# Kernel tuning notes

Hardware: AMD Instinct MI355X
Metric: run time of the kernel (lower is better)

The kernel has to match this reference:

```python
import jax, jax.numpy as jnp
import numpy as np

# NTM hyperparams (must match init_kwargs)
U = 256        # controller units
N = 128        # memory locations
M = 64         # memory vector size
R = 1          # read heads
WH = 1         # write heads
SHIFT = 1      # conv shift range
S = 2 * SHIFT + 1
OUT = 8        # num_bits_per_vector
CLIP = 20.0
IN_DIM = OUT + 1  # copy task input channels
H = R + WH
PER = M + 1 + 1 + S + 1           # k, beta, g, s, gamma per head
P = H * PER + WH * 2 * M          # + erase/add per write head


def setup_inputs() -> dict:
    key = jax.random.key(0)
    ks = jax.random.split(key, 10)
    B, T = 128, 130
    ctrl_in = IN_DIM + R * M
    def gn(k, shape, fan_in):
        return jax.random.normal(k, shape, jnp.float32) / jnp.sqrt(jnp.float32(fan_in))
    return {
        "inputs": (jax.random.uniform(ks[0], (B, T, IN_DIM)) > 0.5).astype(jnp.float32),
        "W_x": gn(ks[1], (ctrl_in, 4 * U), ctrl_in),
        "W_h": gn(ks[2], (U, 4 * U), U),
        "b_lstm": jnp.zeros((4 * U,), jnp.float32),
        "W_p": gn(ks[3], (U, P), U),
        "b_p": jnp.zeros((P,), jnp.float32),
        "W_o": gn(ks[4], (U + R * M, OUT), U + R * M),
        "b_o": jnp.zeros((OUT,), jnp.float32),
        "r0": jax.random.normal(ks[5], (R, M), jnp.float32) * 0.1,
        "w0": jax.random.normal(ks[6], (H, N), jnp.float32) * 0.1,
        "max_seq_len": 64,
    }


def _ntm_forward(inputs, W_x, W_h, b_lstm, W_p, b_p, W_o, b_o, r0, w0):
    B, T, _ = inputs.shape
    # constant-init memory, learned init read vectors / weightings
    Mem0 = jnp.full((B, N, M), 1e-6, jnp.float32)
    r_prev0 = jnp.broadcast_to(jnp.tanh(r0)[None], (B, R, M))
    w_prev0 = jnp.broadcast_to(jax.nn.softmax(w0, axis=-1)[None], (B, H, N))
    h0 = jnp.zeros((B, U), jnp.float32)
    c0 = jnp.zeros((B, U), jnp.float32)

    def step(carry, x_t):
        h, c, r_prev, w_prev, Mem = carry
        # controller LSTM (input = x_t ++ prev read vectors)
        ctrl_in = jnp.concatenate([x_t, r_prev.reshape(B, R * M)], axis=-1)
        gates = ctrl_in @ W_x + h @ W_h + b_lstm
        i, f, g_, o = jnp.split(gates, 4, axis=-1)
        c = jax.nn.sigmoid(f) * c + jax.nn.sigmoid(i) * jnp.tanh(g_)
        h = jax.nn.sigmoid(o) * jnp.tanh(c)
        # head parameters
        params = jnp.clip(h @ W_p + b_p, -CLIP, CLIP)
        hp = params[:, : H * PER].reshape(B, H, PER)
        k = jnp.tanh(hp[..., :M])                              # [B,H,M]
        beta = jax.nn.softplus(hp[..., M])[..., None]          # [B,H,1]
        g = jax.nn.sigmoid(hp[..., M + 1])[..., None]          # [B,H,1]
        s = jax.nn.softmax(hp[..., M + 2 : M + 2 + S], axis=-1)  # [B,H,S]
        gamma = (1.0 + jax.nn.softplus(hp[..., M + 2 + S]))[..., None]  # [B,H,1]
        ea = params[:, H * PER :].reshape(B, WH, 2, M)
        erase = jax.nn.sigmoid(ea[:, :, 0])                    # [B,WH,M]
        add = jnp.tanh(ea[:, :, 1])                            # [B,WH,M]
        # content addressing: cosine similarity
        inner = jnp.einsum("bhm,bnm->bhn", k, Mem)
        kn = jnp.linalg.norm(k, axis=-1, keepdims=True)        # [B,H,1]
        Mn = jnp.linalg.norm(Mem, axis=-1)[:, None, :]         # [B,1,N]
        K = inner / (kn * Mn + 1e-8)
        w_c = jax.nn.softmax(beta * K, axis=-1)                # [B,H,N]
        # interpolation
        w_g = g * w_c + (1.0 - g) * w_prev
        # circular convolutional shift
        w_tilde = jnp.zeros_like(w_g)
        for d in range(-SHIFT, SHIFT + 1):
            w_tilde = w_tilde + s[..., d + SHIFT : d + SHIFT + 1] * jnp.roll(w_g, d, axis=-1)
        # sharpening
        w_pow = w_tilde ** gamma
        w = w_pow / (jnp.sum(w_pow, axis=-1, keepdims=True) + 1e-8)
        w_r, w_w = w[:, :R], w[:, R:]
        # write (sequential over write heads)
        for j in range(WH):
            ww = w_w[:, j, :, None]                            # [B,N,1]
            Mem = Mem * (1.0 - ww * erase[:, j, None, :]) + ww * add[:, j, None, :]
        # read
        r = jnp.einsum("brn,bnm->brm", w_r, Mem)
        out = jnp.clip(jnp.concatenate([h, r.reshape(B, R * M)], axis=-1) @ W_o + b_o, -CLIP, CLIP)
        return (h, c, r, w, Mem), out

    xs = jnp.swapaxes(inputs, 0, 1)  # [T,B,IN]
    _, outs = jax.lax.scan(step, (h0, c0, r_prev0, w_prev0, Mem0), xs)
    return jnp.swapaxes(outs, 0, 1)  # [B,T,OUT]


def reference(inputs, W_x, W_h, b_lstm, W_p, b_p, W_o, b_o, r0, w0, max_seq_len):
    seq = _ntm_forward(inputs, W_x, W_h, b_lstm, W_p, b_p, W_o, b_o, r0, w0)
    logits = seq[:, max_seq_len + 1 :, :]  # copy task slice
    return jax.nn.sigmoid(logits)
```

## Files before the change

kernel.cpp:

```cpp
#include <hip/hip_runtime.h>
#include <math.h>

typedef _Float16 h2_t __attribute__((ext_vector_type(2)));

#define U_ 256
#define NN 128
#define MM 64
#define OUT_ 8
#define CLIPV 20.0f
#define IN_DIM_ 9
#define PP 268
#define B_ 128
#define T_ 130
#define TSTART 65

#define NWXI 6144
#define NWH8 16384
#define NWP8 4352
#define WXI_OFF 0
#define WH8_OFF 98304
#define WP8_OFF 360448
#define BLH_OFF 430080
#define BPP_OFF 434176
#define COMM_OFF 435264
#define COMM_STRIDE 2176
#define COMM_SZ (B_*COMM_STRIDE)
#define PREP_N (NWXI + NWH8 + NWP8 + 256 + 272)

#define WSCALE 256.f
#define HSCALE 127.f
#define OSCALE (1.f/(256.f*127.f))

__device__ __forceinline__ float sigf(float x){ return 1.0f/(1.0f+__expf(-x)); }
__device__ __forceinline__ float splus(float x){ return log1pf(__expf(x)); }
__device__ __forceinline__ float clipf(float x){ return fminf(fmaxf(x,-CLIPV),CLIPV); }

#if defined(__has_builtin)
#if __has_builtin(__builtin_amdgcn_sdot4)
#define SDOT4(a,b,c) __builtin_amdgcn_sdot4((a),(b),(c),false)
#endif
#endif
#ifndef SDOT4
__device__ __forceinline__ int sdot4_sw(int a, int b, int c){
    c += (int)(signed char)(a      ) * (int)(signed char)(b      );
    c += (int)(signed char)(a >> 8 ) * (int)(signed char)(b >> 8 );
    c += (int)(signed char)(a >> 16) * (int)(signed char)(b >> 16);
    c += (a >> 24) * (b >> 24);
    return c;
}
#define SDOT4(a,b,c) sdot4_sw((a),(b),(c))
#endif

#define SD4(u, hw) { \
    a0 = SDOT4((int)(u).x, hw, a0); a1 = SDOT4((int)(u).y, hw, a1); \
    a2 = SDOT4((int)(u).z, hw, a2); a3 = SDOT4((int)(u).w, hw, a3); }
#define SD4P(u, hw) { \
    pa0 = SDOT4((int)(u).x, hw, pa0); pa1 = SDOT4((int)(u).y, hw, pa1); \
    pa2 = SDOT4((int)(u).z, hw, pa2); pa3 = SDOT4((int)(u).w, hw, pa3); }

__device__ __forceinline__ unsigned ei8(float w){
    int v = (int)rintf(w * WSCALE);
    v = v < -127 ? -127 : (v > 127 ? 127 : v);
    return (unsigned)(v & 0xFF);
}

__device__ __forceinline__ unsigned packi8x4(float a, float b, float c, float d){
    int va = (int)rintf(a * HSCALE); va = va < -127 ? -127 : (va > 127 ? 127 : va);
    int vb = (int)rintf(b * HSCALE); vb = vb < -127 ? -127 : (vb > 127 ? 127 : vb);
    int vc = (int)rintf(c * HSCALE); vc = vc < -127 ? -127 : (vc > 127 ? 127 : vc);
    int vd = (int)rintf(d * HSCALE); vd = vd < -127 ? -127 : (vd > 127 ? 127 : vd);
    return (va & 0xFF) | ((vb & 0xFF) << 8) | ((vc & 0xFF) << 16) | ((vd & 0xFF) << 24);
}

__global__ void prep_kernel(const float* __restrict__ W_x, const float* __restrict__ W_h,
                            const float* __restrict__ W_p, const float* __restrict__ b_lstm,
                            const float* __restrict__ b_p,
                            uint4* __restrict__ wxi8, uint4* __restrict__ whi8,
                            uint4* __restrict__ wpi8,
                            float4* __restrict__ blh, float* __restrict__ bpp)
{
    for (int idx = blockIdx.x*blockDim.x + threadIdx.x; idx < PREP_N; idx += gridDim.x*blockDim.x){
        if (idx < NWXI){
            int hf = idx/3072, rem = idx - hf*3072;
            int wv = rem/192, r2 = rem - wv*192, j = r2>>6, ln = r2&63;
            int g4 = wv*8 + (ln>>3), q = ln&7, kb = q*12 + 4*j;
            unsigned c[4];
            #pragma unroll
            for (int g=0; g<4; ++g){
                int col = g*256 + hf*128 + g4;
                unsigned w = 0;
                #pragma unroll
                for (int k=0; k<4; ++k){
                    int K = kb+k;
                    float f = (K<64) ? W_x[(9+K)*1024+col] : (K<73 ? W_x[(K-64)*1024+col] : 0.f);
                    w |= ei8(f) << (8*k);
                }
                c[g] = w;
            }
            wxi8[idx] = make_uint4(c[0],c[1],c[2],c[3]);
        } else if (idx < NWXI + NWH8){
            int e = idx - NWXI;
            int hf = e>>13, rem = e&8191, g4 = rem>>6, s = rem&63;
            int j = s>>3, q = s&7, kb = q*32 + 4*j;
            unsigned c[4];
            #pragma unroll
            for (int g=0; g<4; ++g){
                int col = g*256 + hf*128 + g4;
                c[g] = ei8(W_h[(kb+0)*1024+col])
                     | (ei8(W_h[(kb+1)*1024+col]) << 8)
                     | (ei8(W_h[(kb+2)*1024+col]) << 16)
                     | (ei8(W_h[(kb+3)*1024+col]) << 24);
            }
            whi8[e] = make_uint4(c[0],c[1],c[2],c[3]);
        } else if (idx < NWXI + NWH8 + NWP8){
            int e = idx - NWXI - NWH8;
            int cg = e>>6, s = e&63;
            int j = s>>3, q = s&7, kb = q*32 + 4*j;
            unsigned c[4];
            #pragma unroll
            for (int g=0; g<4; ++g){
                int cl = cg*4+g;
                if (cl < PP){
                    c[g] = ei8(W_p[(kb+0)*PP+cl])
                         | (ei8(W_p[(kb+1)*PP+cl]) << 8)
                         | (ei8(W_p[(kb+2)*PP+cl]) << 16)
                         | (ei8(W_p[(kb+3)*PP+cl]) << 24);
                } else c[g] = 0u;
            }
            wpi8[e] = make_uint4(c[0],c[1],c[2],c[3]);
        } else if (idx < NWXI + NWH8 + NWP8 + 256){
            int u = idx - NWXI - NWH8 - NWP8;
            blh[u] = make_float4(b_lstm[u], b_lstm[256+u], b_lstm[512+u], b_lstm[768+u]);
        } else {
            int j = idx - NWXI - NWH8 - NWP8 - 256;
            bpp[j] = (j < PP) ? b_p[j] : 0.f;
        }
    }
}

__device__ __forceinline__ float decodeP(int rc, float p){
    if (rc < 64 || (rc >= 70 && rc < 134) || rc >= 204) return tanhf(p);
    if (rc >= 140 && rc < 204) return sigf(p);
    return p;
}

__global__ __launch_bounds__(1024,1) void ntm_kernel(
    const float* __restrict__ inputs,
    const float* __restrict__ W_o, const float* __restrict__ b_o,
    const float* __restrict__ r0, const float* __restrict__ w0,
    const uint4* __restrict__ wxi8, const uint4* __restrict__ whi8,
    const uint4* __restrict__ wpi8,
    const float4* __restrict__ blh, const float* __restrict__ bpp,
    char* comm, float* __restrict__ out)
{
    const int bid = blockIdx.x, hf = bid>>7, b = bid&127;
    const int t = threadIdx.x, wv = t>>6, ln = t&63;
    const int g4 = t>>3, q = t&7;

    char* cb = comm + b*COMM_STRIDE;
    volatile float* hOwn = (volatile float*)(cb + hf*512);
    volatile float* hOth = (volatile float*)(cb + (hf^1)*512);
    volatile int*   flg  = (volatile int*)(cb + 2112);

    __shared__ uint4 wxL8[3072];
    __shared__ uint4 whL8[4][1024];
    __shared__ float Mem[NN][MM+1];
    __shared__ float4 gpart4[128];
    __shared__ float4 blhL[128];
    __shared__ float hbuf[U_];
    __shared__ float cbuf[128];
    __shared__ unsigned hq[64];
    __shared__ unsigned xq[24];
    __shared__ float prmS[12];
    __shared__ float scal[12];
    __shared__ float kv[2][MM], ebuf[MM], abuf[MM];
    __shared__ float innr[2][NN], Mn[NN], wgs[2][NN], wtab[2][NN];
    __shared__ float rpart[16][MM];
    __shared__ float jpart[OUT_];

    for (int i=t; i<3072; i+=1024) wxL8[i] = wxi8[hf*3072 + i];
    for (int i=t; i<4096; i+=1024){
        int j = i>>10, jj = i&1023;
        whL8[j][jj] = whi8[hf*8192 + (jj>>3)*64 + j*8 + (jj&7)];
    }
    for (int i=t; i<NN*MM; i+=1024) Mem[i>>6][i&63] = 1e-6f;
    if (t < 128){
        gpart4[t] = make_float4(0.f,0.f,0.f,0.f);
        blhL[t] = blh[hf*128+t];
        cbuf[t] = 0.f;
        Mn[t] = 8e-6f;
    }
    if (t < 64) hq[t] = 0u;
    if (t < U_) hbuf[t] = 0.f;
    if (t >= 128 && t < 256){
        int h = (t-128)>>6, l = t&63;
        float v0 = w0[h*NN + l], v1 = w0[h*NN + l + 64];
        float mx = fmaxf(v0,v1);
        for (int off=32; off>=1; off>>=1) mx = fmaxf(mx, __shfl_xor(mx, off));
        float e0 = __expf(v0-mx), e1 = __expf(v1-mx);
        float s = e0+e1;
        for (int off=32; off>=1; off>>=1) s += __shfl_xor(s, off);
        wtab[h][l] = e0/s; wtab[h][l+64] = e1/s;
    }
    if (t >= 256 && t < 280){
        int p = t-256;
        if (p < 16){
            xq[p] = packi8x4(tanhf(r0[4*p]), tanhf(r0[4*p+1]), tanhf(r0[4*p+2]), tanhf(r0[4*p+3]));
        } else if (p < 19){
            const float* xin = inputs + b*T_*IN_DIM_;
            int e0 = 4*(p-16);
            float f0 = (e0+0<IN_DIM_) ? xin[e0+0] : 0.f;
            float f1 = (e0+1<IN_DIM_) ? xin[e0+1] : 0.f;
            float f2 = (e0+2<IN_DIM_) ? xin[e0+2] : 0.f;
            float f3 = (e0+3<IN_DIM_) ? xin[e0+3] : 0.f;
            xq[p] = packi8x4(f0,f1,f2,f3);
        } else xq[p] = 0u;
    }
    __syncthreads();

    for (int step=0; step<T_; ++step){
        const int* xqi = (const int*)xq;

        {
            const uint4* wb = wxL8 + wv*192;
            int a0=0,a1=0,a2=0,a3=0;
            #pragma unroll
            for (int j=0; j<3; ++j){
                uint4 u = wb[j*64 + ln];
                int xw = xqi[q*3+j];
                SD4(u, xw);
            }
            #pragma unroll
            for (int m=1; m<8; m<<=1){
                a0 += __shfl_xor(a0,m); a1 += __shfl_xor(a1,m);
                a2 += __shfl_xor(a2,m); a3 += __shfl_xor(a3,m);
            }
            if (q==0){
                float4 bb = blhL[g4]; float4 gp = gpart4[g4];
                float gi=a0*OSCALE+bb.x+gp.x, gf=a1*OSCALE+bb.y+gp.y;
                float gg=a2*OSCALE+bb.z+gp.z, go=a3*OSCALE+bb.w+gp.w;
                float c = sigf(gf)*cbuf[g4] + sigf(gi)*tanhf(gg);
                cbuf[g4] = c;
                float h = sigf(go)*tanhf(c);
                hbuf[hf*128+g4] = h;
                hOwn[g4] = h;
            }
        }
        __syncthreads();
        if (t==0){
            flg[hf] = step+1;
            while (flg[hf^1] < step+1) __builtin_amdgcn_s_sleep(2);
        }
        __syncthreads();
        if (t < 128){
            hbuf[(hf^1)*128 + t] = hOth[t];
        } else if (t < 160){
            const int jj = t-128;
            const float* hp = &hbuf[hf*128 + 4*jj];
            hq[hf*32 + jj] = packi8x4(hp[0], hp[1], hp[2], hp[3]);
        } else if (t < 192){
            const int jj = t-160;
            float h0 = hOth[4*jj], h1 = hOth[4*jj+1], h2 = hOth[4*jj+2], h3 = hOth[4*jj+3];
            hq[(hf^1)*32 + jj] = packi8x4(h0, h1, h2, h3);
        }
        __syncthreads();

        const int* hqi = (const int*)hq;

        {
            const uint4* wrow = whi8 + hf*8192 + g4*64;
            int a0=0,a1=0,a2=0,a3=0;
            uint4 s4 = wrow[32+q], s5 = wrow[40+q], s6 = wrow[48+q], s7 = wrow[56+q];
            uint4 l0 = whL8[0][t], l1 = whL8[1][t], l2 = whL8[2][t], l3 = whL8[3][t];
            int hw0=hqi[q*8+0], hw1=hqi[q*8+1], hw2=hqi[q*8+2], hw3=hqi[q*8+3];
            int hw4=hqi[q*8+4], hw5=hqi[q*8+5], hw6=hqi[q*8+6], hw7=hqi[q*8+7];
            SD4(l0, hw0); SD4(l1, hw1);
            SD4(l2, hw2); SD4(l3, hw3);
            SD4(s4, hw4); SD4(s5, hw5);
            SD4(s6, hw6); SD4(s7, hw7);
            #pragma unroll
            for (int m=1; m<8; m<<=1){
                a0 += __shfl_xor(a0,m); a1 += __shfl_xor(a1,m);
                a2 += __shfl_xor(a2,m); a3 += __shfl_xor(a3,m);
            }
            if (q==0) gpart4[g4] = make_float4(a0*OSCALE, a1*OSCALE, a2*OSCALE, a3*OSCALE);
        }
        if (t < 544){
            const int cg = t>>3, qq = t&7;
            const uint4* wrow = wpi8 + cg*64;
            int pa0=0, pa1=0, pa2=0, pa3=0;
            uint4 u0=wrow[0*8+qq], u1=wrow[1*8+qq], u2=wrow[2*8+qq], u3=wrow[3*8+qq];
            uint4 u4=wrow[4*8+qq], u5=wrow[5*8+qq], u6=wrow[6*8+qq], u7=wrow[7*8+qq];
            int hw0=hqi[qq*8+0], hw1=hqi[qq*8+1], hw2=hqi[qq*8+2], hw3=hqi[qq*8+3];
            int hw4=hqi[qq*8+4], hw5=hqi[qq*8+5], hw6=hqi[qq*8+6], hw7=hqi[qq*8+7];
            SD4P(u0, hw0); SD4P(u1, hw1);
            SD4P(u2, hw2); SD4P(u3, hw3);
            SD4P(u4, hw4); SD4P(u5, hw5);
            SD4P(u6, hw6); SD4P(u7, hw7);
            #pragma unroll
            for (int m=1; m<8; m<<=1){
                pa0 += __shfl_xor(pa0,m); pa1 += __shfl_xor(pa1,m);
                pa2 += __shfl_xor(pa2,m); pa3 += __shfl_xor(pa3,m);
            }
            if (qq==0){
                #pragma unroll
                for (int j=0; j<4; ++j){
                    int aj = (j==0)?pa0:((j==1)?pa1:((j==2)?pa2:pa3));
                    int cl = cg*4+j;
                    if (cl < PP){
                        float pv = clipf(aj*OSCALE + bpp[cl]);
                        float dv = decodeP(cl, pv);
                        if (cl < 64) kv[0][cl] = dv;
                        else if (cl < 70) prmS[cl-64] = dv;
                        else if (cl < 134) kv[1][cl-70] = dv;
                        else if (cl < 140) prmS[6+cl-134] = dv;
                        else if (cl < 204) ebuf[cl-140] = dv;
                        else abuf[cl-204] = dv;
                    }
                }
            }
        } else if (t < 800){
            const int idx = t-544, n = idx>>1, m0 = (idx&1)*32;
            float s = 0.f;
            #pragma unroll 8
            for (int m=m0; m<m0+32; ++m){ float v=Mem[n][m]; s=fmaf(v,v,s); }
            s += __shfl_xor(s,1);
            if (!(idx&1)) Mn[n] = sqrtf(s);
        } else if (t < 928){
            const int o = (t-800)>>4, l16 = (t-800)&15;
            float s = 0.f;
            #pragma unroll
            for (int j=0; j<16; ++j){
                const int i = l16 + (j<<4);
                s = fmaf(hbuf[i], W_o[i*OUT_ + o], s);
            }
            s += __shfl_xor(s,1); s += __shfl_xor(s,2);
            s += __shfl_xor(s,4); s += __shfl_xor(s,8);
            if (l16==0) jpart[o] = s;
        } else if (t < 931){
            if (step+1 < T_){
                const int p = t-928;
                const float* xin = inputs + (b*T_ + step+1)*IN_DIM_;
                int e0 = 4*p;
                float f0 = (e0+0<IN_DIM_) ? xin[e0+0] : 0.f;
                float f1 = (e0+1<IN_DIM_) ? xin[e0+1] : 0.f;
                float f2 = (e0+2<IN_DIM_) ? xin[e0+2] : 0.f;
                float f3 = (e0+3<IN_DIM_) ? xin[e0+3] : 0.f;
                xq[16+p] = packi8x4(f0,f1,f2,f3);
            }
        }
        __syncthreads();

        {
            const int h = t>>9, n = (t>>2)&127, qm = t&3, m0 = qm*16;
            float s = 0.f;
            #pragma unroll 8
            for (int m=m0; m<m0+16; ++m) s = fmaf(kv[h][m], Mem[n][m], s);
            s += __shfl_xor(s,1); s += __shfl_xor(s,2);
            if (qm==0) innr[h][n] = s;
        }
        if (t < 2){
            const int h = t;
            const float* ps = prmS + 6*h;
            scal[h]   = splus(ps[0]);
            scal[2+h] = sigf(ps[1]);
            float p0=ps[2], p1=ps[3], p2=ps[4];
            float mx = fmaxf(p0, fmaxf(p1, p2));
            float e0=__expf(p0-mx), e1=__expf(p1-mx), e2=__expf(p2-mx);
            float s = e0+e1+e2;
            scal[6+3*h]=e0/s; scal[7+3*h]=e1/s; scal[8+3*h]=e2/s;
            scal[4+h] = 1.f + splus(ps[5]);
        }
        __syncthreads();

        if (t < 128){
            const int h = t>>6, l = ln;
            float kvl = kv[h][l];
            float kn2 = kvl*kvl;
            for (int off=32; off>=1; off>>=1) kn2 += __shfl_xor(kn2, off);
            float kn = sqrtf(kn2);
            float beta = scal[h], g = scal[2+h];
            float bk0 = beta * innr[h][l]   /(kn*Mn[l]   +1e-8f);
            float bk1 = beta * innr[h][l+64]/(kn*Mn[l+64]+1e-8f);
            float mx = fmaxf(bk0,bk1);
            for (int off=32; off>=1; off>>=1) mx = fmaxf(mx, __shfl_xor(mx, off));
            float e0=__expf(bk0-mx), e1=__expf(bk1-mx);
            float s=e0+e1;
            for (int off=32; off>=1; off>>=1) s += __shfl_xor(s, off);
            float wc0=e0/s, wc1=e1/s;
            wgs[h][l]    = g*wc0 + (1.f-g)*wtab[h][l];
            wgs[h][l+64] = g*wc1 + (1.f-g)*wtab[h][l+64];
            float gamma = scal[4+h];
            float s0=scal[6+3*h], s1=scal[7+3*h], s2=scal[8+3*h];
            const int n0=l, n1=l+64;
            float wt0 = s0*wgs[h][(n0+1)&127] + s1*wgs[h][n0] + s2*wgs[h][(n0+127)&127];
            float wt1 = s0*wgs[h][(n1+1)&127] + s1*wgs[h][n1] + s2*wgs[h][(n1+127)&127];
            float wp0 = __powf(wt0, gamma), wp1 = __powf(wt1, gamma);
            float ss = wp0+wp1;
            for (int off=32; off>=1; off>>=1) ss += __shfl_xor(ss, off);
            float inv = 1.0f/(ss+1e-8f);
            wtab[h][n0] = wp0*inv; wtab[h][n1] = wp1*inv;
        }
        __syncthreads();

        {
            const float el = ebuf[ln], al = abuf[ln];
            const int n0 = wv*8;
            float racc = 0.f;
            #pragma unroll
            for (int k=0; k<8; ++k){
                const int n = n0+k;
                float ww = wtab[1][n];
                float wr = wtab[0][n];
                float v = Mem[n][ln]*(1.0f - ww*el) + ww*al;
                Mem[n][ln] = v;
                racc = fmaf(wr, v, racc);
            }
            rpart[wv][ln] = racc;
        }
        __syncthreads();

        if (t < 512){
            const int o = wv;
            float rm = 0.f;
            #pragma unroll
            for (int k=0; k<16; ++k) rm += rpart[k][ln];
            float s = rm * W_o[(U_+ln)*OUT_ + o];
            for (int off=32; off>=1; off>>=1) s += __shfl_xor(s, off);
            if (ln==0 && hf==0 && step>=TSTART){
                float logit = clipf(s + jpart[o] + b_o[o]);
                out[((b*(T_-TSTART)) + (step-TSTART))*OUT_ + o] = sigf(logit);
            }
        } else if (t < 576){
            float rm = 0.f;
            #pragma unroll
            for (int k=0; k<16; ++k) rm += rpart[k][ln];
            float r1 = __shfl_down(rm, 1);
            float r2 = __shfl_down(rm, 2);
            float r3 = __shfl_down(rm, 3);
            if (!(ln&3)) xq[ln>>2] = packi8x4(rm, r1, r2, r3);
        }
        __syncthreads();
    }
}

extern "C" void kernel_launch(void* const* d_in, const int* in_sizes, int n_in,
                              void* d_out, int out_size, void* d_ws, size_t ws_size,
                              hipStream_t stream) {
    const float* inputs = (const float*)d_in[0];
    const float* W_x    = (const float*)d_in[1];
    const float* W_h    = (const float*)d_in[2];
    const float* b_lstm = (const float*)d_in[3];
    const float* W_p    = (const float*)d_in[4];
    const float* b_p    = (const float*)d_in[5];
    const float* W_o    = (const float*)d_in[6];
    const float* b_o    = (const float*)d_in[7];
    const float* r0     = (const float*)d_in[8];
    const float* w0     = (const float*)d_in[9];
    float* out = (float*)d_out;

    char* ws = (char*)d_ws;
    uint4*  wxi = (uint4*)(ws + WXI_OFF);
    uint4*  wh8 = (uint4*)(ws + WH8_OFF);
    uint4*  wp8 = (uint4*)(ws + WP8_OFF);
    float4* blh = (float4*)(ws + BLH_OFF);
    float*  bpp = (float*)(ws + BPP_OFF);
    char*   comm = ws + COMM_OFF;

    hipMemsetAsync(comm, 0, COMM_SZ, stream);
    prep_kernel<<<512, 256, 0, stream>>>(W_x, W_h, W_p, b_lstm, b_p, wxi, wh8, wp8, blh, bpp);
    ntm_kernel<<<2*B_, 1024, 0, stream>>>(inputs, W_o, b_o, r0, w0,
                                          wxi, wh8, wp8, blh, bpp, comm, out);
}
```

Measured before the change: 1.559 ms.

## Keep memory matrix in registers and cache more W_h rows in LDS

```diff
diff --git a/kernel.cpp b/kernel.cpp
--- a/kernel.cpp
+++ b/kernel.cpp
@@ -163,8 +163,7 @@
     volatile int*   flg  = (volatile int*)(cb + 2112);
 
     __shared__ uint4 wxL8[3072];
-    __shared__ uint4 whL8[4][1024];
-    __shared__ float Mem[NN][MM+1];
+    __shared__ uint4 whL8[6][1024];
     __shared__ float4 gpart4[128];
     __shared__ float4 blhL[128];
     __shared__ float hbuf[U_];
@@ -178,12 +177,15 @@
     __shared__ float rpart[16][MM];
     __shared__ float jpart[OUT_];
 
+    float memR[8];
+    #pragma unroll
+    for (int k=0; k<8; ++k) memR[k] = 1e-6f;
+
     for (int i=t; i<3072; i+=1024) wxL8[i] = wxi8[hf*3072 + i];
-    for (int i=t; i<4096; i+=1024){
+    for (int i=t; i<6144; i+=1024){
         int j = i>>10, jj = i&1023;
         whL8[j][jj] = whi8[hf*8192 + (jj>>3)*64 + j*8 + (jj&7)];
     }
-    for (int i=t; i<NN*MM; i+=1024) Mem[i>>6][i&63] = 1e-6f;
     if (t < 128){
         gpart4[t] = make_float4(0.f,0.f,0.f,0.f);
         blhL[t] = blh[hf*128+t];
@@ -270,13 +272,14 @@
         {
             const uint4* wrow = whi8 + hf*8192 + g4*64;
             int a0=0,a1=0,a2=0,a3=0;
-            uint4 s4 = wrow[32+q], s5 = wrow[40+q], s6 = wrow[48+q], s7 = wrow[56+q];
-            uint4 l0 = whL8[0][t], l1 = whL8[1][t], l2 = whL8[2][t], l3 = whL8[3][t];
+            uint4 s6 = wrow[48+q], s7 = wrow[56+q];
+            uint4 l0 = whL8[0][t], l1 = whL8[1][t], l2 = whL8[2][t];
+            uint4 l3 = whL8[3][t], l4 = whL8[4][t], l5 = whL8[5][t];
             int hw0=hqi[q*8+0], hw1=hqi[q*8+1], hw2=hqi[q*8+2], hw3=hqi[q*8+3];
             int hw4=hqi[q*8+4], hw5=hqi[q*8+5], hw6=hqi[q*8+6], hw7=hqi[q*8+7];
             SD4(l0, hw0); SD4(l1, hw1);
             SD4(l2, hw2); SD4(l3, hw3);
-            SD4(s4, hw4); SD4(s5, hw5);
+            SD4(l4, hw4); SD4(l5, hw5);
             SD4(s6, hw6); SD4(s7, hw7);
             #pragma unroll
             for (int m=1; m<8; m<<=1){
@@ -319,14 +322,7 @@
                     }
                 }
             }
-        } else if (t < 800){
-            const int idx = t-544, n = idx>>1, m0 = (idx&1)*32;
-            float s = 0.f;
-            #pragma unroll 8
-            for (int m=m0; m<m0+32; ++m){ float v=Mem[n][m]; s=fmaf(v,v,s); }
-            s += __shfl_xor(s,1);
-            if (!(idx&1)) Mn[n] = sqrtf(s);
-        } else if (t < 928){
+        } else if (t >= 800 && t < 928){
             const int o = (t-800)>>4, l16 = (t-800)&15;
             float s = 0.f;
             #pragma unroll
@@ -337,7 +333,7 @@
             s += __shfl_xor(s,1); s += __shfl_xor(s,2);
             s += __shfl_xor(s,4); s += __shfl_xor(s,8);
             if (l16==0) jpart[o] = s;
-        } else if (t < 931){
+        } else if (t >= 928 && t < 931){
             if (step+1 < T_){
                 const int p = t-928;
                 const float* xin = inputs + (b*T_ + step+1)*IN_DIM_;
@@ -352,12 +348,20 @@
         __syncthreads();
 
         {
-            const int h = t>>9, n = (t>>2)&127, qm = t&3, m0 = qm*16;
-            float s = 0.f;
-            #pragma unroll 8
-            for (int m=m0; m<m0+16; ++m) s = fmaf(kv[h][m], Mem[n][m], s);
-            s += __shfl_xor(s,1); s += __shfl_xor(s,2);
-            if (qm==0) innr[h][n] = s;
+            float k0l = kv[0][ln], k1l = kv[1][ln];
+            #pragma unroll
+            for (int k=0; k<8; ++k){
+                const int n = wv*8 + k;
+                float m = memR[k];
+                float s0 = k0l*m, s1 = k1l*m, s2 = m*m;
+                #pragma unroll
+                for (int off=32; off>=1; off>>=1){
+                    s0 += __shfl_xor(s0,off);
+                    s1 += __shfl_xor(s1,off);
+                    s2 += __shfl_xor(s2,off);
+                }
+                if (ln==0){ innr[0][n]=s0; innr[1][n]=s1; Mn[n]=sqrtf(s2); }
+            }
         }
         if (t < 2){
             const int h = t;
@@ -405,15 +409,14 @@
 
         {
             const float el = ebuf[ln], al = abuf[ln];
-            const int n0 = wv*8;
             float racc = 0.f;
             #pragma unroll
             for (int k=0; k<8; ++k){
-                const int n = n0+k;
+                const int n = wv*8 + k;
                 float ww = wtab[1][n];
                 float wr = wtab[0][n];
-                float v = Mem[n][ln]*(1.0f - ww*el) + ww*al;
-                Mem[n][ln] = v;
+                float v = memR[k]*(1.0f - ww*el) + ww*al;
+                memR[k] = v;
                 racc = fmaf(wr, v, racc);
             }
             rpart[wv][ln] = racc;
```

New measurement: 2.297 ms. +47.4%, slower.
